# Optimization experiments

Measured on AMD Instinct MI355X. Metric: run time of the kernel, lower is better.

The kernel has to match this reference:

```python
import jax, jax.numpy as jnp
import numpy as np

NUM_EMB = 1000
HIDDEN = 256
SCALE = 2
N_HEADS = 8
HEAD_DIM = HIDDEN * SCALE // N_HEADS  # 64
HS = HIDDEN * SCALE  # 512
EPS = 1e-6


def setup_inputs() -> dict:
    key = jax.random.key(0)
    ks = jax.random.split(key, 12)
    B, N, C, H, W = 8, 8, HIDDEN, 32, 32
    std = 0.02
    return {
        "q": jax.random.randint(ks[0], (B,), 0, NUM_EMB, dtype=jnp.int32),
        "c": jax.random.normal(ks[1], (B, N, C, H, W), dtype=jnp.float32),
        "rms_w": jnp.ones((HIDDEN,), dtype=jnp.float32),
        "emb": jax.random.normal(ks[2], (NUM_EMB, HIDDEN), dtype=jnp.float32) * std,
        "w1": jax.random.normal(ks[3], (HIDDEN, HS), dtype=jnp.float32) * std,
        "b1": jnp.zeros((HS,), dtype=jnp.float32),
        "w2": jax.random.normal(ks[4], (HS, HS), dtype=jnp.float32) * std,
        "b2": jnp.zeros((HS,), dtype=jnp.float32),
        "w_kv": jax.random.normal(ks[5], (HIDDEN, HS * 2), dtype=jnp.float32) * std,
        "w_out": jax.random.normal(ks[6], (HS, HIDDEN), dtype=jnp.float32) * std,
        "b_out": jnp.zeros((HIDDEN,), dtype=jnp.float32),
    }


def reference(q, c, rms_w, emb, w1, b1, w2, b2, w_kv, w_out, b_out):
    B, N, C, H, W = c.shape
    attn_scale = HEAD_DIM ** (-0.5)
    # permute to [B,H,W,N,C] and RMSNorm over channel dim
    c = jnp.transpose(c, (0, 3, 4, 1, 2))
    c = c * jax.lax.rsqrt(jnp.mean(c * c, axis=-1, keepdims=True) + EPS) * rms_w
    # query path: embed + gated MLP -> [B, n_heads, head_dim]
    qe = emb[q]                                   # [B, hidden]
    qh = jax.nn.silu(qe @ w1 + b1) @ w2 + b2      # [B, HS]
    qh = qh.reshape(B, N_HEADS, HEAD_DIM)
    # kv projection: [B,H,W,N, 2*HS] -> [B,H,W,n_heads,N, 2*head_dim]
    kv = (c @ w_kv).reshape(B, H, W, N, N_HEADS, 2 * HEAD_DIM)
    kv = jnp.transpose(kv, (0, 1, 2, 4, 3, 5))
    k, v = jnp.split(kv, 2, axis=-1)              # each [B,H,W,heads,N,head_dim]
    # broadcast per-pixel cross-attention: query shared over H,W
    dots = jnp.einsum('bed,bhwend->bhwen', qh, k) * attn_scale
    attn = jax.nn.softmax(dots, axis=-1)
    h = jnp.einsum('bhwen,bhwend->bhwed', attn, v)  # [B,H,W,heads,head_dim]
    h = h.reshape(B, H, W, HS)
    out = h @ w_out + b_out                        # [B,H,W,hidden]
    return jnp.transpose(out, (0, 3, 1, 2))        # [B,hidden,H,W]
```

## Files before the change

kernel.cpp:

```cpp
#include <hip/hip_runtime.h>

typedef _Float16 f16;
typedef _Float16 f16x8 __attribute__((ext_vector_type(8)));
typedef float f32x4 __attribute__((ext_vector_type(4)));

static __device__ inline char* a_addr(char* Abase, int px, int k) {
    return Abase + px * 4096 + ((((k >> 3) ^ (px & 15)) << 4) | ((k & 7) << 1));
}

__launch_bounds__(256)
__global__ void k_setup(const int* __restrict__ q, const float* __restrict__ emb,
                        const float* __restrict__ w1, const float* __restrict__ b1,
                        const float* __restrict__ w2, const float* __restrict__ b2,
                        const float* __restrict__ w_kv, const float* __restrict__ w_out,
                        const float* __restrict__ rms_w,
                        f16* __restrict__ qkw, f16* __restrict__ mtp) {
    int blk = blockIdx.x;
    int t = threadIdx.x;
    __shared__ float qe[256];
    __shared__ float x1L[512];
    __shared__ float ps[4][64];
    __shared__ float qhL[64];
    __shared__ float wv[64][8];

    if (blk < 64) {
        int b = blk >> 3, e = blk & 7;
        qe[t] = emb[(size_t)q[b] * 256 + t];
        __syncthreads();
        float a0 = b1[t], a1 = b1[t + 256];
#pragma unroll 4
        for (int c = 0; c < 256; ++c) {
            float qv = qe[c];
            a0 += qv * w1[c * 512 + t];
            a1 += qv * w1[c * 512 + t + 256];
        }
        x1L[t]       = a0 / (1.f + __expf(-a0));
        x1L[t + 256] = a1 / (1.f + __expf(-a1));
        __syncthreads();
        int d = t & 63, ks = t >> 6;
        float acc = 0.f;
#pragma unroll 4
        for (int k = ks * 128; k < ks * 128 + 128; ++k)
            acc += x1L[k] * w2[k * 512 + e * 64 + d];
        ps[ks][d] = acc;
        __syncthreads();
        if (t < 64)
            qhL[t] = b2[e * 64 + t] + ps[0][t] + ps[1][t] + ps[2][t] + ps[3][t];
        __syncthreads();
        const float* row = w_kv + (size_t)t * 1024 + e * 128;
        float a2 = 0.f;
#pragma unroll
        for (int dd = 0; dd < 64; dd += 4) {
            float4 wv4 = *(const float4*)(row + dd);
            a2 += qhL[dd] * wv4.x + qhL[dd + 1] * wv4.y + qhL[dd + 2] * wv4.z + qhL[dd + 3] * wv4.w;
        }
        qkw[(b * 8 + e) * 256 + t] = (f16)(a2 * rms_w[t]);
    } else {
        int mb = blk - 64;
        int e = mb >> 5, c0 = (mb & 31) * 8;
        {
            int d = t & 63, cc = t >> 6;
            wv[d][cc]     = w_kv[(size_t)(c0 + cc) * 1024 + e * 128 + 64 + d];
            wv[d][cc + 4] = w_kv[(size_t)(c0 + cc + 4) * 1024 + e * 128 + 64 + d];
        }
        __syncthreads();
        int o = t;
        float acc[8];
#pragma unroll
        for (int c = 0; c < 8; ++c) acc[c] = 0.f;
#pragma unroll 4
        for (int d = 0; d < 64; ++d) {
            float wo = w_out[(size_t)(e * 64 + d) * 256 + o];
            float4 wa = *(const float4*)&wv[d][0];
            float4 wb = *(const float4*)&wv[d][4];
            acc[0] += wa.x * wo; acc[1] += wa.y * wo; acc[2] += wa.z * wo; acc[3] += wa.w * wo;
            acc[4] += wb.x * wo; acc[5] += wb.y * wo; acc[6] += wb.z * wo; acc[7] += wb.w * wo;
        }
        f16x8 ov;
#pragma unroll
        for (int c = 0; c < 8; ++c) ov[c] = (f16)(acc[c] * rms_w[c0 + c]);
        *(f16x8*)(mtp + ((size_t)((e * 256 + c0) >> 3) * 256 + o) * 8) = ov;
    }
}

__launch_bounds__(1024, 4)
__global__ void k_attn(const float* __restrict__ cin, const f16* __restrict__ qkw,
                       const f16* __restrict__ mtp, const float* __restrict__ b_out,
                       float* __restrict__ out) {
    int blk = blockIdx.x;
    int b = blk & 7;
    int hw0 = (blk >> 3) * 32;
    int t = threadIdx.x;
    int lane = t & 63, w = t >> 6;
    int m16 = lane & 15, quad = lane >> 4;
    int half = lane >> 5;

    __shared__ char A[32 * 4096];
    __shared__ float dotsP[8][8][32];
    __shared__ float wred[16][8][32];
    __shared__ float rinvL[32][8];

    int px = lane & 31;
    int cb = w + half * 16;
    const float* cbase = cin + ((size_t)b * 8 * 256) * 1024 + hw0 + px;
#pragma unroll
    for (int g = 0; g < 8; g += 2) {
        const float* s0 = cbase + ((size_t)(g * 256 + cb * 8) << 10);
        const float* s1 = cbase + ((size_t)((g + 1) * 256 + cb * 8) << 10);
        float v0[8], v1[8];
#pragma unroll
        for (int j = 0; j < 8; ++j) v0[j] = s0[(size_t)j << 10];
#pragma unroll
        for (int j = 0; j < 8; ++j) v1[j] = s1[(size_t)j << 10];
        float sa = 0.f, sb = 0.f;
        f16x8 h0, h1;
#pragma unroll
        for (int j = 0; j < 8; ++j) { sa += v0[j] * v0[j]; h0[j] = (f16)v0[j]; }
#pragma unroll
        for (int j = 0; j < 8; ++j) { sb += v1[j] * v1[j]; h1[j] = (f16)v1[j]; }
        *(f16x8*)a_addr(A, px, g * 256 + cb * 8)       = h0;
        *(f16x8*)a_addr(A, px, (g + 1) * 256 + cb * 8) = h1;
        sa += __shfl_xor(sa, 32);
        sb += __shfl_xor(sb, 32);
        if (lane < 32) {
            wred[w][g][px]     = sa;
            wred[w][g + 1][px] = sb;
        }
    }
    __syncthreads();

    if (t < 256) {
        int p = t >> 3, n = t & 7;
        float ss = 0.f;
#pragma unroll
        for (int ww = 0; ww < 16; ++ww) ss += wred[ww][n][p];
        rinvL[p][n] = rsqrtf(ss * (1.f / 256.f) + 1e-6f);
    }
    {
        int n = w & 7, pxh = w >> 3;
        f32x4 d0 = {0.f, 0.f, 0.f, 0.f};
        const f16* qrow = qkw + (size_t)b * 2048 + (m16 & 7) * 256;
#pragma unroll
        for (int ks = 0; ks < 8; ++ks) {
            f16x8 a0  = *(const f16x8*)a_addr(A, pxh * 16 + m16, n * 256 + ks * 32 + quad * 8);
            f16x8 bfr = *(const f16x8*)(qrow + ks * 32 + quad * 8);
            d0 = __builtin_amdgcn_mfma_f32_16x16x32_f16(a0, bfr, d0, 0, 0, 0);
        }
        if (m16 < 8) {
#pragma unroll
            for (int r = 0; r < 4; ++r) dotsP[n][m16][pxh * 16 + quad * 4 + r] = d0[r];
        }
    }
    __syncthreads();

    int o = w * 16 + m16;
    f16x8 pb[8];
#pragma unroll
    for (int ks = 0; ks < 8; ++ks)
        pb[ks] = *(const f16x8*)(mtp + ((size_t)(ks * 4 + quad) * 256 + o) * 8);

    {
        int bpx = lane & 31;
        int c0 = (w + half * 16) * 8;
        float rinv[8];
#pragma unroll
        for (int n = 0; n < 8; ++n) rinv[n] = rinvL[bpx][n];
        f16x8 cv[8];
#pragma unroll
        for (int n = 0; n < 8; ++n)
            cv[n] = *(const f16x8*)a_addr(A, bpx, n * 256 + c0);
#pragma unroll
        for (int e = 0; e < 8; ++e) {
            float l[8];
#pragma unroll
            for (int n = 0; n < 8; ++n) l[n] = dotsP[n][e][bpx] * rinv[n] * 0.125f;
            float mx = l[0];
#pragma unroll
            for (int n = 1; n < 8; ++n) mx = fmaxf(mx, l[n]);
            float s = 0.f;
#pragma unroll
            for (int n = 0; n < 8; ++n) { l[n] = __expf(l[n] - mx); s += l[n]; }
            float inv = 1.f / s;
            f16x8 r = {};
#pragma unroll
            for (int n = 0; n < 8; ++n) {
                f16 an = (f16)(l[n] * inv * rinv[n]);
#pragma unroll
                for (int j = 0; j < 8; ++j) r[j] += cv[n][j] * an;
            }
            *(f16x8*)a_addr(A, bpx, e * 256 + c0) = r;
        }
    }
    __syncthreads();

    {
        f32x4 acc0 = {0.f, 0.f, 0.f, 0.f};
        f32x4 acc1 = {0.f, 0.f, 0.f, 0.f};
#pragma unroll
        for (int ks = 0; ks < 8; ++ks) {
            int k = ks * 32 + quad * 8;
            f16x8 af0 = *(const f16x8*)a_addr(A, m16, k);
            f16x8 af1 = *(const f16x8*)a_addr(A, m16 + 16, k);
            acc0 = __builtin_amdgcn_mfma_f32_16x16x32_f16(af0, pb[ks], acc0, 0, 0, 0);
            acc1 = __builtin_amdgcn_mfma_f32_16x16x32_f16(af1, pb[ks], acc1, 0, 0, 0);
        }
#pragma unroll 8
        for (int ks = 8; ks < 64; ++ks) {
            int k = (ks >> 3) * 256 + (ks & 7) * 32 + quad * 8;
            int kchunk = k >> 3;
            f16x8 bfr = *(const f16x8*)(mtp + ((size_t)kchunk * 256 + o) * 8);
            f16x8 af0 = *(const f16x8*)a_addr(A, m16, k);
            f16x8 af1 = *(const f16x8*)a_addr(A, m16 + 16, k);
            acc0 = __builtin_amdgcn_mfma_f32_16x16x32_f16(af0, bfr, acc0, 0, 0, 0);
            acc1 = __builtin_amdgcn_mfma_f32_16x16x32_f16(af1, bfr, acc1, 0, 0, 0);
        }
        float bo = b_out[o];
        float* drow = out + ((size_t)b * 256 + o) * 1024 + hw0;
        float4 v0 = {acc0[0] + bo, acc0[1] + bo, acc0[2] + bo, acc0[3] + bo};
        float4 v1 = {acc1[0] + bo, acc1[1] + bo, acc1[2] + bo, acc1[3] + bo};
        *(float4*)(drow + quad * 4)      = v0;
        *(float4*)(drow + 16 + quad * 4) = v1;
    }
}

extern "C" void kernel_launch(void* const* d_in, const int* in_sizes, int n_in,
                              void* d_out, int out_size, void* d_ws, size_t ws_size,
                              hipStream_t stream) {
    (void)in_sizes; (void)n_in; (void)out_size; (void)ws_size;
    const int*   q     = (const int*)d_in[0];
    const float* c     = (const float*)d_in[1];
    const float* rms_w = (const float*)d_in[2];
    const float* emb   = (const float*)d_in[3];
    const float* w1    = (const float*)d_in[4];
    const float* b1    = (const float*)d_in[5];
    const float* w2    = (const float*)d_in[6];
    const float* b2    = (const float*)d_in[7];
    const float* w_kv  = (const float*)d_in[8];
    const float* w_out = (const float*)d_in[9];
    const float* b_out = (const float*)d_in[10];
    float* out = (float*)d_out;

    char* ws = (char*)d_ws;
    f16* qkw = (f16*)ws;
    f16* mtp = (f16*)(ws + 32768);

    k_setup<<<320, 256, 0, stream>>>(q, emb, w1, b1, w2, b2, w_kv, w_out, rms_w, qkw, mtp);
    k_attn <<<256, 1024, 0, stream>>>(c, qkw, mtp, b_out, out);
}
```

Before: 166.2 us.

## Halve attention pixel tile to 16 and double grid to 512 blocks

```diff
diff --git a/kernel.cpp b/kernel.cpp
--- a/kernel.cpp
+++ b/kernel.cpp
@@ -1,6 +1,7 @@
 #include <hip/hip_runtime.h>
 
 typedef _Float16 f16;
+typedef _Float16 f16x4 __attribute__((ext_vector_type(4)));
 typedef _Float16 f16x8 __attribute__((ext_vector_type(8)));
 typedef float f32x4 __attribute__((ext_vector_type(4)));
 
@@ -83,92 +84,80 @@
     }
 }
 
-__launch_bounds__(1024, 4)
+__launch_bounds__(1024, 8)
 __global__ void k_attn(const float* __restrict__ cin, const f16* __restrict__ qkw,
                        const f16* __restrict__ mtp, const float* __restrict__ b_out,
                        float* __restrict__ out) {
     int blk = blockIdx.x;
     int b = blk & 7;
-    int hw0 = (blk >> 3) * 32;
+    int hw0 = (blk >> 3) * 16;
     int t = threadIdx.x;
     int lane = t & 63, w = t >> 6;
     int m16 = lane & 15, quad = lane >> 4;
-    int half = lane >> 5;
-
-    __shared__ char A[32 * 4096];
-    __shared__ float dotsP[8][8][32];
-    __shared__ float wred[16][8][32];
-    __shared__ float rinvL[32][8];
-
-    int px = lane & 31;
-    int cb = w + half * 16;
-    const float* cbase = cin + ((size_t)b * 8 * 256) * 1024 + hw0 + px;
-#pragma unroll
-    for (int g = 0; g < 8; g += 2) {
-        const float* s0 = cbase + ((size_t)(g * 256 + cb * 8) << 10);
-        const float* s1 = cbase + ((size_t)((g + 1) * 256 + cb * 8) << 10);
-        float v0[8], v1[8];
-#pragma unroll
-        for (int j = 0; j < 8; ++j) v0[j] = s0[(size_t)j << 10];
-#pragma unroll
-        for (int j = 0; j < 8; ++j) v1[j] = s1[(size_t)j << 10];
-        float sa = 0.f, sb = 0.f;
-        f16x8 h0, h1;
-#pragma unroll
-        for (int j = 0; j < 8; ++j) { sa += v0[j] * v0[j]; h0[j] = (f16)v0[j]; }
-#pragma unroll
-        for (int j = 0; j < 8; ++j) { sb += v1[j] * v1[j]; h1[j] = (f16)v1[j]; }
-        *(f16x8*)a_addr(A, px, g * 256 + cb * 8)       = h0;
-        *(f16x8*)a_addr(A, px, (g + 1) * 256 + cb * 8) = h1;
-        sa += __shfl_xor(sa, 32);
-        sb += __shfl_xor(sb, 32);
-        if (lane < 32) {
-            wred[w][g][px]     = sa;
-            wred[w][g + 1][px] = sb;
-        }
+
+    __shared__ char A[16 * 4096];
+    __shared__ float dotsP[8][8][16];
+    __shared__ float wred[16][16];
+    __shared__ float rinvL[16][9];
+
+    {
+        int px = m16;
+        int cb = (w << 2) | quad;
+        const float* src = cin + ((size_t)b * 2048 + (size_t)cb * 32) * 1024 + hw0 + px;
+        float ss = 0.f;
+#pragma unroll
+        for (int jb = 0; jb < 4; jb += 2) {
+            float v0[8], v1[8];
+#pragma unroll
+            for (int j = 0; j < 8; ++j) v0[j] = src[(size_t)(jb * 8 + j) << 10];
+#pragma unroll
+            for (int j = 0; j < 8; ++j) v1[j] = src[(size_t)(jb * 8 + 8 + j) << 10];
+            f16x8 h0, h1;
+#pragma unroll
+            for (int j = 0; j < 8; ++j) { ss += v0[j] * v0[j]; h0[j] = (f16)v0[j]; }
+#pragma unroll
+            for (int j = 0; j < 8; ++j) { ss += v1[j] * v1[j]; h1[j] = (f16)v1[j]; }
+            *(f16x8*)a_addr(A, px, cb * 32 + jb * 8)     = h0;
+            *(f16x8*)a_addr(A, px, cb * 32 + jb * 8 + 8) = h1;
+        }
+        ss += __shfl_xor(ss, 16);
+        ss += __shfl_xor(ss, 32);
+        if (lane < 16) wred[w][lane] = ss;
     }
     __syncthreads();
 
-    if (t < 256) {
-        int p = t >> 3, n = t & 7;
-        float ss = 0.f;
-#pragma unroll
-        for (int ww = 0; ww < 16; ++ww) ss += wred[ww][n][p];
-        rinvL[p][n] = rsqrtf(ss * (1.f / 256.f) + 1e-6f);
-    }
-    {
-        int n = w & 7, pxh = w >> 3;
+    if (w < 8) {
+        int n = w;
         f32x4 d0 = {0.f, 0.f, 0.f, 0.f};
         const f16* qrow = qkw + (size_t)b * 2048 + (m16 & 7) * 256;
 #pragma unroll
         for (int ks = 0; ks < 8; ++ks) {
-            f16x8 a0  = *(const f16x8*)a_addr(A, pxh * 16 + m16, n * 256 + ks * 32 + quad * 8);
-            f16x8 bfr = *(const f16x8*)(qrow + ks * 32 + quad * 8);
-            d0 = __builtin_amdgcn_mfma_f32_16x16x32_f16(a0, bfr, d0, 0, 0, 0);
+            f16x8 a0 = *(const f16x8*)a_addr(A, m16, n * 256 + ks * 32 + quad * 8);
+            f16x8 bq = *(const f16x8*)(qrow + ks * 32 + quad * 8);
+            d0 = __builtin_amdgcn_mfma_f32_16x16x32_f16(a0, bq, d0, 0, 0, 0);
         }
         if (m16 < 8) {
 #pragma unroll
-            for (int r = 0; r < 4; ++r) dotsP[n][m16][pxh * 16 + quad * 4 + r] = d0[r];
-        }
+            for (int r = 0; r < 4; ++r) dotsP[n][m16][quad * 4 + r] = d0[r];
+        }
+    } else if (w < 10) {
+        int i = t - 512;
+        int p = i & 15, n = i >> 4;
+        float ss = wred[2 * n][p] + wred[2 * n + 1][p];
+        rinvL[p][n] = rsqrtf(ss * (1.f / 256.f) + 1e-6f);
     }
     __syncthreads();
 
-    int o = w * 16 + m16;
-    f16x8 pb[8];
-#pragma unroll
-    for (int ks = 0; ks < 8; ++ks)
-        pb[ks] = *(const f16x8*)(mtp + ((size_t)(ks * 4 + quad) * 256 + o) * 8);
-
     {
-        int bpx = lane & 31;
-        int c0 = (w + half * 16) * 8;
+        int bpx = t & 15;
+        int cw = t >> 4;
         float rinv[8];
 #pragma unroll
         for (int n = 0; n < 8; ++n) rinv[n] = rinvL[bpx][n];
-        f16x8 cv[8];
+        f16x4 cv[8];
 #pragma unroll
         for (int n = 0; n < 8; ++n)
-            cv[n] = *(const f16x8*)a_addr(A, bpx, n * 256 + c0);
+            cv[n] = *(const f16x4*)a_addr(A, bpx, n * 256 + cw * 4);
 #pragma unroll
         for (int e = 0; e < 8; ++e) {
             float l[8];
@@ -181,45 +170,32 @@
 #pragma unroll
             for (int n = 0; n < 8; ++n) { l[n] = __expf(l[n] - mx); s += l[n]; }
             float inv = 1.f / s;
-            f16x8 r = {};
+            f16x4 r = {};
 #pragma unroll
             for (int n = 0; n < 8; ++n) {
                 f16 an = (f16)(l[n] * inv * rinv[n]);
 #pragma unroll
-                for (int j = 0; j < 8; ++j) r[j] += cv[n][j] * an;
+                for (int j = 0; j < 4; ++j) r[j] += cv[n][j] * an;
             }
-            *(f16x8*)a_addr(A, bpx, e * 256 + c0) = r;
+            *(f16x4*)a_addr(A, bpx, e * 256 + cw * 4) = r;
         }
     }
     __syncthreads();
 
     {
-        f32x4 acc0 = {0.f, 0.f, 0.f, 0.f};
-        f32x4 acc1 = {0.f, 0.f, 0.f, 0.f};
-#pragma unroll
-        for (int ks = 0; ks < 8; ++ks) {
+        int o = (w << 4) | m16;
+        float bo = b_out[o];
+        f32x4 acc = {0.f, 0.f, 0.f, 0.f};
+#pragma unroll 4
+        for (int ks = 0; ks < 64; ++ks) {
             int k = ks * 32 + quad * 8;
-            f16x8 af0 = *(const f16x8*)a_addr(A, m16, k);
-            f16x8 af1 = *(const f16x8*)a_addr(A, m16 + 16, k);
-            acc0 = __builtin_amdgcn_mfma_f32_16x16x32_f16(af0, pb[ks], acc0, 0, 0, 0);
-            acc1 = __builtin_amdgcn_mfma_f32_16x16x32_f16(af1, pb[ks], acc1, 0, 0, 0);
-        }
-#pragma unroll 8
-        for (int ks = 8; ks < 64; ++ks) {
-            int k = (ks >> 3) * 256 + (ks & 7) * 32 + quad * 8;
-            int kchunk = k >> 3;
-            f16x8 bfr = *(const f16x8*)(mtp + ((size_t)kchunk * 256 + o) * 8);
-            f16x8 af0 = *(const f16x8*)a_addr(A, m16, k);
-            f16x8 af1 = *(const f16x8*)a_addr(A, m16 + 16, k);
-            acc0 = __builtin_amdgcn_mfma_f32_16x16x32_f16(af0, bfr, acc0, 0, 0, 0);
-            acc1 = __builtin_amdgcn_mfma_f32_16x16x32_f16(af1, bfr, acc1, 0, 0, 0);
-        }
-        float bo = b_out[o];
+            f16x8 bfr = *(const f16x8*)(mtp + ((size_t)(ks * 4 + quad) * 256 + o) * 8);
+            f16x8 af  = *(const f16x8*)a_addr(A, m16, k);
+            acc = __builtin_amdgcn_mfma_f32_16x16x32_f16(af, bfr, acc, 0, 0, 0);
+        }
         float* drow = out + ((size_t)b * 256 + o) * 1024 + hw0;
-        float4 v0 = {acc0[0] + bo, acc0[1] + bo, acc0[2] + bo, acc0[3] + bo};
-        float4 v1 = {acc1[0] + bo, acc1[1] + bo, acc1[2] + bo, acc1[3] + bo};
-        *(float4*)(drow + quad * 4)      = v0;
-        *(float4*)(drow + 16 + quad * 4) = v1;
+        float4 v0 = {acc[0] + bo, acc[1] + bo, acc[2] + bo, acc[3] + bo};
+        *(float4*)(drow + quad * 4) = v0;
     }
 }
 
@@ -245,5 +221,5 @@
     f16* mtp = (f16*)(ws + 32768);
 
     k_setup<<<320, 256, 0, stream>>>(q, emb, w1, b1, w2, b2, w_kv, w_out, rms_w, qkw, mtp);
-    k_attn <<<256, 1024, 0, stream>>>(c, qkw, mtp, b_out, out);
-}
+    k_attn <<<512, 1024, 0, stream>>>(c, qkw, mtp, b_out, out);
+}
```

After: 178.2 us. +7.2%, slower.

## Deduplicate query MLP per batch and precompute softmax weights once per pixel

Applied to the files above, without the earlier changes.

```diff
diff --git a/kernel.cpp b/kernel.cpp
--- a/kernel.cpp
+++ b/kernel.cpp
@@ -1,6 +1,7 @@
 #include <hip/hip_runtime.h>
 
 typedef _Float16 f16;
+typedef _Float16 f16x4 __attribute__((ext_vector_type(4)));
 typedef _Float16 f16x8 __attribute__((ext_vector_type(8)));
 typedef float f32x4 __attribute__((ext_vector_type(4)));
 
@@ -8,7 +9,7 @@
     return Abase + px * 4096 + ((((k >> 3) ^ (px & 15)) << 4) | ((k & 7) << 1));
 }
 
-__launch_bounds__(256)
+__launch_bounds__(1024)
 __global__ void k_setup(const int* __restrict__ q, const float* __restrict__ emb,
                         const float* __restrict__ w1, const float* __restrict__ b1,
                         const float* __restrict__ w2, const float* __restrict__ b2,
@@ -17,62 +18,85 @@
                         f16* __restrict__ qkw, f16* __restrict__ mtp) {
     int blk = blockIdx.x;
     int t = threadIdx.x;
-    __shared__ float qe[256];
-    __shared__ float x1L[512];
-    __shared__ float ps[4][64];
-    __shared__ float qhL[64];
-    __shared__ float wv[64][8];
-
-    if (blk < 64) {
-        int b = blk >> 3, e = blk & 7;
-        qe[t] = emb[(size_t)q[b] * 256 + t];
-        __syncthreads();
-        float a0 = b1[t], a1 = b1[t + 256];
-#pragma unroll 4
-        for (int c = 0; c < 256; ++c) {
-            float qv = qe[c];
-            a0 += qv * w1[c * 512 + t];
-            a1 += qv * w1[c * 512 + t + 256];
-        }
-        x1L[t]       = a0 / (1.f + __expf(-a0));
-        x1L[t + 256] = a1 / (1.f + __expf(-a1));
-        __syncthreads();
-        int d = t & 63, ks = t >> 6;
-        float acc = 0.f;
-#pragma unroll 4
-        for (int k = ks * 128; k < ks * 128 + 128; ++k)
-            acc += x1L[k] * w2[k * 512 + e * 64 + d];
-        ps[ks][d] = acc;
-        __syncthreads();
-        if (t < 64)
-            qhL[t] = b2[e * 64 + t] + ps[0][t] + ps[1][t] + ps[2][t] + ps[3][t];
-        __syncthreads();
-        const float* row = w_kv + (size_t)t * 1024 + e * 128;
-        float a2 = 0.f;
-#pragma unroll
-        for (int dd = 0; dd < 64; dd += 4) {
-            float4 wv4 = *(const float4*)(row + dd);
-            a2 += qhL[dd] * wv4.x + qhL[dd + 1] * wv4.y + qhL[dd + 2] * wv4.z + qhL[dd + 3] * wv4.w;
-        }
-        qkw[(b * 8 + e) * 256 + t] = (f16)(a2 * rms_w[t]);
+
+    if (blk < 8) {
+        int b = blk;
+        __shared__ float qe[256];
+        __shared__ float x1[512];
+        __shared__ float qh[512];
+        __shared__ float psA[1024];
+        __shared__ float psB[1024];
+
+        if (t < 256) qe[t] = emb[(size_t)q[b] * 256 + t];
+        __syncthreads();
+
+        {
+            int h = t & 511, half = t >> 9;
+            float acc = half ? 0.f : b1[h];
+            int c0 = half * 128;
+#pragma unroll 8
+            for (int c = c0; c < c0 + 128; ++c)
+                acc += qe[c] * w1[(size_t)c * 512 + h];
+            psA[half * 512 + h] = acc;
+        }
+        __syncthreads();
+        if (t < 512) {
+            float a = psA[t] + psA[512 + t];
+            x1[t] = a / (1.f + __expf(-a));
+        }
+        __syncthreads();
+
+        {
+            int o = t & 511, half = t >> 9;
+            float acc = half ? 0.f : b2[o];
+            int k0 = half * 256;
+#pragma unroll 8
+            for (int k = k0; k < k0 + 256; ++k)
+                acc += x1[k] * w2[(size_t)k * 512 + o];
+            psB[half * 512 + o] = acc;
+        }
+        __syncthreads();
+        if (t < 512) qh[t] = psB[t] + psB[512 + t];
+        __syncthreads();
+
+        {
+            int c = t & 255, g = t >> 8;
+            float rw = rms_w[c];
+#pragma unroll
+            for (int ee = 0; ee < 2; ++ee) {
+                int e = g * 2 + ee;
+                const float* col = w_kv + (size_t)c * 1024 + e * 128;
+                float acc = 0.f;
+#pragma unroll
+                for (int dq = 0; dq < 16; ++dq) {
+                    float4 wv4 = *(const float4*)(col + dq * 4);
+                    const float* qb = &qh[e * 64 + dq * 4];
+                    acc += wv4.x * qb[0] + wv4.y * qb[1]
+                         + wv4.z * qb[2] + wv4.w * qb[3];
+                }
+                qkw[((size_t)b * 8 + e) * 256 + c] = (f16)(acc * rw);
+            }
+        }
     } else {
-        int mb = blk - 64;
+        __shared__ float wv[4][64][8];
+        int sub = t >> 8, st = t & 255;
+        int mb = (blk - 8) * 4 + sub;
         int e = mb >> 5, c0 = (mb & 31) * 8;
         {
-            int d = t & 63, cc = t >> 6;
-            wv[d][cc]     = w_kv[(size_t)(c0 + cc) * 1024 + e * 128 + 64 + d];
-            wv[d][cc + 4] = w_kv[(size_t)(c0 + cc + 4) * 1024 + e * 128 + 64 + d];
-        }
-        __syncthreads();
-        int o = t;
+            int d = st & 63, cc = st >> 6;
+            wv[sub][d][cc]     = w_kv[(size_t)(c0 + cc) * 1024 + e * 128 + 64 + d];
+            wv[sub][d][cc + 4] = w_kv[(size_t)(c0 + cc + 4) * 1024 + e * 128 + 64 + d];
+        }
+        __syncthreads();
+        int o = st;
         float acc[8];
 #pragma unroll
         for (int c = 0; c < 8; ++c) acc[c] = 0.f;
 #pragma unroll 4
         for (int d = 0; d < 64; ++d) {
             float wo = w_out[(size_t)(e * 64 + d) * 256 + o];
-            float4 wa = *(const float4*)&wv[d][0];
-            float4 wb = *(const float4*)&wv[d][4];
+            float4 wa = *(const float4*)&wv[sub][d][0];
+            float4 wb = *(const float4*)&wv[sub][d][4];
             acc[0] += wa.x * wo; acc[1] += wa.y * wo; acc[2] += wa.z * wo; acc[3] += wa.w * wo;
             acc[4] += wb.x * wo; acc[5] += wb.y * wo; acc[6] += wb.z * wo; acc[7] += wb.w * wo;
         }
@@ -97,8 +121,11 @@
 
     __shared__ char A[32 * 4096];
     __shared__ float dotsP[8][8][32];
-    __shared__ float wred[16][8][32];
+    __shared__ char pool[16384];
     __shared__ float rinvL[32][8];
+
+    float* wredF = (float*)pool;
+    f16*   attnH = (f16*)pool;
 
     int px = lane & 31;
     int cb = w + half * 16;
@@ -123,8 +150,8 @@
         sa += __shfl_xor(sa, 32);
         sb += __shfl_xor(sb, 32);
         if (lane < 32) {
-            wred[w][g][px]     = sa;
-            wred[w][g + 1][px] = sb;
+            wredF[w * 256 + g * 32 + px]       = sa;
+            wredF[w * 256 + (g + 1) * 32 + px] = sb;
         }
     }
     __syncthreads();
@@ -133,7 +160,7 @@
         int p = t >> 3, n = t & 7;
         float ss = 0.f;
 #pragma unroll
-        for (int ww = 0; ww < 16; ++ww) ss += wred[ww][n][p];
+        for (int ww = 0; ww < 16; ++ww) ss += wredF[ww * 256 + n * 32 + p];
         rinvL[p][n] = rsqrtf(ss * (1.f / 256.f) + 1e-6f);
     }
     {
@@ -159,32 +186,41 @@
     for (int ks = 0; ks < 8; ++ks)
         pb[ks] = *(const f16x8*)(mtp + ((size_t)(ks * 4 + quad) * 256 + o) * 8);
 
+    if (t < 256) {
+        int e = t >> 5, p = t & 31;
+        float rv[8], l[8];
+#pragma unroll
+        for (int n = 0; n < 8; ++n) rv[n] = rinvL[p][n];
+#pragma unroll
+        for (int n = 0; n < 8; ++n) l[n] = dotsP[n][e][p] * rv[n] * 0.125f;
+        float mx = l[0];
+#pragma unroll
+        for (int n = 1; n < 8; ++n) mx = fmaxf(mx, l[n]);
+        float s = 0.f;
+#pragma unroll
+        for (int n = 0; n < 8; ++n) { l[n] = __expf(l[n] - mx); s += l[n]; }
+        float inv = 1.f / s;
+        f16x8 av;
+#pragma unroll
+        for (int n = 0; n < 8; ++n) av[n] = (f16)(l[n] * inv * rv[n]);
+        *(f16x8*)(attnH + e * 256 + p * 8) = av;
+    }
+    __syncthreads();
+
     {
         int bpx = lane & 31;
         int c0 = (w + half * 16) * 8;
-        float rinv[8];
-#pragma unroll
-        for (int n = 0; n < 8; ++n) rinv[n] = rinvL[bpx][n];
         f16x8 cv[8];
 #pragma unroll
         for (int n = 0; n < 8; ++n)
             cv[n] = *(const f16x8*)a_addr(A, bpx, n * 256 + c0);
 #pragma unroll
         for (int e = 0; e < 8; ++e) {
-            float l[8];
-#pragma unroll
-            for (int n = 0; n < 8; ++n) l[n] = dotsP[n][e][bpx] * rinv[n] * 0.125f;
-            float mx = l[0];
-#pragma unroll
-            for (int n = 1; n < 8; ++n) mx = fmaxf(mx, l[n]);
-            float s = 0.f;
-#pragma unroll
-            for (int n = 0; n < 8; ++n) { l[n] = __expf(l[n] - mx); s += l[n]; }
-            float inv = 1.f / s;
+            f16x8 av = *(const f16x8*)(attnH + e * 256 + bpx * 8);
             f16x8 r = {};
 #pragma unroll
             for (int n = 0; n < 8; ++n) {
-                f16 an = (f16)(l[n] * inv * rinv[n]);
+                f16 an = av[n];
 #pragma unroll
                 for (int j = 0; j < 8; ++j) r[j] += cv[n][j] * an;
             }
@@ -244,6 +280,6 @@
     f16* qkw = (f16*)ws;
     f16* mtp = (f16*)(ws + 32768);
 
-    k_setup<<<320, 256, 0, stream>>>(q, emb, w1, b1, w2, b2, w_kv, w_out, rms_w, qkw, mtp);
+    k_setup<<<72, 1024, 0, stream>>>(q, emb, w1, b1, w2, b2, w_kv, w_out, rms_w, qkw, mtp);
     k_attn <<<256, 1024, 0, stream>>>(c, qkw, mtp, b_out, out);
 }
```

After: 171.8 us. +3.3%, slower.

## Make the input load wave-local and compute softmax once per pixel-head

Applied to the files above, without the earlier changes.

```diff
diff --git a/kernel.cpp b/kernel.cpp
--- a/kernel.cpp
+++ b/kernel.cpp
@@ -1,6 +1,7 @@
 #include <hip/hip_runtime.h>
 
 typedef _Float16 f16;
+typedef _Float16 f16x4 __attribute__((ext_vector_type(4)));
 typedef _Float16 f16x8 __attribute__((ext_vector_type(8)));
 typedef float f32x4 __attribute__((ext_vector_type(4)));
 
@@ -97,54 +98,41 @@
 
     __shared__ char A[32 * 4096];
     __shared__ float dotsP[8][8][32];
-    __shared__ float wred[16][8][32];
-    __shared__ float rinvL[32][8];
-
-    int px = lane & 31;
-    int cb = w + half * 16;
-    const float* cbase = cin + ((size_t)b * 8 * 256) * 1024 + hw0 + px;
-#pragma unroll
-    for (int g = 0; g < 8; g += 2) {
-        const float* s0 = cbase + ((size_t)(g * 256 + cb * 8) << 10);
-        const float* s1 = cbase + ((size_t)((g + 1) * 256 + cb * 8) << 10);
-        float v0[8], v1[8];
-#pragma unroll
-        for (int j = 0; j < 8; ++j) v0[j] = s0[(size_t)j << 10];
-#pragma unroll
-        for (int j = 0; j < 8; ++j) v1[j] = s1[(size_t)j << 10];
-        float sa = 0.f, sb = 0.f;
-        f16x8 h0, h1;
-#pragma unroll
-        for (int j = 0; j < 8; ++j) { sa += v0[j] * v0[j]; h0[j] = (f16)v0[j]; }
-#pragma unroll
-        for (int j = 0; j < 8; ++j) { sb += v1[j] * v1[j]; h1[j] = (f16)v1[j]; }
-        *(f16x8*)a_addr(A, px, g * 256 + cb * 8)       = h0;
-        *(f16x8*)a_addr(A, px, (g + 1) * 256 + cb * 8) = h1;
-        sa += __shfl_xor(sa, 32);
-        sb += __shfl_xor(sb, 32);
-        if (lane < 32) {
-            wred[w][g][px]     = sa;
-            wred[w][g + 1][px] = sb;
-        }
-    }
-    __syncthreads();
-
-    if (t < 256) {
-        int p = t >> 3, n = t & 7;
+    __shared__ float wredS[16][16];
+    __shared__ f16  attnH[8 * 32 * 8];
+
+    int n = w & 7, pxh = w >> 3;
+    int px = pxh * 16 + m16;
+    {
+        const float* cb0 = cin + (((size_t)b * 2048) << 10) + hw0 + px;
+        int chb = n * 256 + quad * 64;
         float ss = 0.f;
 #pragma unroll
-        for (int ww = 0; ww < 16; ++ww) ss += wred[ww][n][p];
-        rinvL[p][n] = rsqrtf(ss * (1.f / 256.f) + 1e-6f);
-    }
-    {
-        int n = w & 7, pxh = w >> 3;
+        for (int g = 0; g < 4; ++g) {
+            float v[16];
+#pragma unroll
+            for (int j = 0; j < 16; ++j)
+                v[j] = cb0[(size_t)(chb + g * 16 + j) << 10];
+            f16x8 h0, h1;
+#pragma unroll
+            for (int j = 0; j < 8; ++j) { ss += v[j] * v[j]; h0[j] = (f16)v[j]; }
+#pragma unroll
+            for (int j = 0; j < 8; ++j) { float x = v[8 + j]; ss += x * x; h1[j] = (f16)x; }
+            *(f16x8*)a_addr(A, px, chb + g * 16)     = h0;
+            *(f16x8*)a_addr(A, px, chb + g * 16 + 8) = h1;
+        }
+        ss += __shfl_xor(ss, 16);
+        ss += __shfl_xor(ss, 32);
+        if (lane < 16) wredS[w][m16] = ss;
+    }
+    {
         f32x4 d0 = {0.f, 0.f, 0.f, 0.f};
         const f16* qrow = qkw + (size_t)b * 2048 + (m16 & 7) * 256;
 #pragma unroll
         for (int ks = 0; ks < 8; ++ks) {
-            f16x8 a0  = *(const f16x8*)a_addr(A, pxh * 16 + m16, n * 256 + ks * 32 + quad * 8);
-            f16x8 bfr = *(const f16x8*)(qrow + ks * 32 + quad * 8);
-            d0 = __builtin_amdgcn_mfma_f32_16x16x32_f16(a0, bfr, d0, 0, 0, 0);
+            f16x8 a0 = *(const f16x8*)a_addr(A, px, n * 256 + ks * 32 + quad * 8);
+            f16x8 bq = *(const f16x8*)(qrow + ks * 32 + quad * 8);
+            d0 = __builtin_amdgcn_mfma_f32_16x16x32_f16(a0, bq, d0, 0, 0, 0);
         }
         if (m16 < 8) {
 #pragma unroll
@@ -159,34 +147,45 @@
     for (int ks = 0; ks < 8; ++ks)
         pb[ks] = *(const f16x8*)(mtp + ((size_t)(ks * 4 + quad) * 256 + o) * 8);
 
+    if (t < 256) {
+        int e = t >> 5, p = t & 31;
+        int ph = p >> 4, pl = p & 15;
+        float rv[8], l[8];
+#pragma unroll
+        for (int nn = 0; nn < 8; ++nn)
+            rv[nn] = rsqrtf(wredS[ph * 8 + nn][pl] * (1.f / 256.f) + 1e-6f);
+#pragma unroll
+        for (int nn = 0; nn < 8; ++nn) l[nn] = dotsP[nn][e][p] * rv[nn] * 0.125f;
+        float mx = l[0];
+#pragma unroll
+        for (int nn = 1; nn < 8; ++nn) mx = fmaxf(mx, l[nn]);
+        float s = 0.f;
+#pragma unroll
+        for (int nn = 0; nn < 8; ++nn) { l[nn] = __expf(l[nn] - mx); s += l[nn]; }
+        float inv = 1.f / s;
+        f16x8 av;
+#pragma unroll
+        for (int nn = 0; nn < 8; ++nn) av[nn] = (f16)(l[nn] * inv * rv[nn]);
+        *(f16x8*)(attnH + e * 256 + p * 8) = av;
+    }
+    __syncthreads();
+
     {
         int bpx = lane & 31;
         int c0 = (w + half * 16) * 8;
-        float rinv[8];
-#pragma unroll
-        for (int n = 0; n < 8; ++n) rinv[n] = rinvL[bpx][n];
         f16x8 cv[8];
 #pragma unroll
-        for (int n = 0; n < 8; ++n)
-            cv[n] = *(const f16x8*)a_addr(A, bpx, n * 256 + c0);
+        for (int nn = 0; nn < 8; ++nn)
+            cv[nn] = *(const f16x8*)a_addr(A, bpx, nn * 256 + c0);
 #pragma unroll
         for (int e = 0; e < 8; ++e) {
-            float l[8];
-#pragma unroll
-            for (int n = 0; n < 8; ++n) l[n] = dotsP[n][e][bpx] * rinv[n] * 0.125f;
-            float mx = l[0];
-#pragma unroll
-            for (int n = 1; n < 8; ++n) mx = fmaxf(mx, l[n]);
-            float s = 0.f;
-#pragma unroll
-            for (int n = 0; n < 8; ++n) { l[n] = __expf(l[n] - mx); s += l[n]; }
-            float inv = 1.f / s;
+            f16x8 av = *(const f16x8*)(attnH + e * 256 + bpx * 8);
             f16x8 r = {};
 #pragma unroll
-            for (int n = 0; n < 8; ++n) {
-                f16 an = (f16)(l[n] * inv * rinv[n]);
-#pragma unroll
-                for (int j = 0; j < 8; ++j) r[j] += cv[n][j] * an;
+            for (int nn = 0; nn < 8; ++nn) {
+                f16 an = av[nn];
+#pragma unroll
+                for (int j = 0; j < 8; ++j) r[j] += cv[nn][j] * an;
             }
             *(f16x8*)a_addr(A, bpx, e * 256 + c0) = r;
         }
```

Result: no change. 168.0 us (+1.1%).
